# Kernel optimization log

Hardware: AMD Instinct MI355X
Metric: run time of the kernel (lower is better)

## Reference

```python
import jax, jax.numpy as jnp
import numpy as np

N, E, H, NODE_IN, EDGE_DIM, L = 10000, 400000, 128, 6, 3, 4
LN_EPS = 1e-5


def _lin_init(key, fan_in, fan_out):
    return jax.random.normal(key, (fan_in, fan_out), dtype=jnp.float32) / np.sqrt(fan_in)


def setup_inputs() -> dict:
    key = jax.random.key(0)
    ks = jax.random.split(key, 24)
    x = jax.random.normal(ks[0], (N, NODE_IN), dtype=jnp.float32)
    edge_index = jax.random.randint(ks[1], (2, E), 0, N, dtype=jnp.int64)
    edge_attr = jax.random.normal(ks[2], (E, EDGE_DIM), dtype=jnp.float32)
    # encoder
    enc_w1 = _lin_init(ks[3], NODE_IN, H); enc_b1 = jnp.zeros((H,), jnp.float32)
    enc_w2 = _lin_init(ks[4], H, H); enc_b2 = jnp.zeros((H,), jnp.float32)
    # per-layer stacked params [L, ...]
    msg_w1 = jax.vmap(lambda k: _lin_init(k, 2 * H + EDGE_DIM, H))(jax.random.split(ks[5], L))
    msg_b1 = jnp.zeros((L, H), jnp.float32)
    msg_w2 = jax.vmap(lambda k: _lin_init(k, H, H))(jax.random.split(ks[6], L))
    msg_b2 = jnp.zeros((L, H), jnp.float32)
    upd_w1 = jax.vmap(lambda k: _lin_init(k, 2 * H, H))(jax.random.split(ks[7], L))
    upd_b1 = jnp.zeros((L, H), jnp.float32)
    upd_w2 = jax.vmap(lambda k: _lin_init(k, H, H))(jax.random.split(ks[8], L))
    upd_b2 = jnp.zeros((L, H), jnp.float32)
    ln_g = jnp.ones((L, H), jnp.float32)
    ln_b = jnp.zeros((L, H), jnp.float32)
    # decoder
    dec_w1 = _lin_init(ks[9], H, H); dec_b1 = jnp.zeros((H,), jnp.float32)
    dec_w2 = _lin_init(ks[10], H, 1); dec_b2 = jnp.zeros((1,), jnp.float32)
    return dict(x=x, edge_index=edge_index, edge_attr=edge_attr,
                enc_w1=enc_w1, enc_b1=enc_b1, enc_w2=enc_w2, enc_b2=enc_b2,
                msg_w1=msg_w1, msg_b1=msg_b1, msg_w2=msg_w2, msg_b2=msg_b2,
                upd_w1=upd_w1, upd_b1=upd_b1, upd_w2=upd_w2, upd_b2=upd_b2,
                ln_g=ln_g, ln_b=ln_b,
                dec_w1=dec_w1, dec_b1=dec_b1, dec_w2=dec_w2, dec_b2=dec_b2)


def _layernorm(h, g, b):
    mu = jnp.mean(h, axis=-1, keepdims=True)
    var = jnp.mean(jnp.square(h - mu), axis=-1, keepdims=True)
    return (h - mu) * jax.lax.rsqrt(var + LN_EPS) * g + b


def reference(x, edge_index, edge_attr,
              enc_w1, enc_b1, enc_w2, enc_b2,
              msg_w1, msg_b1, msg_w2, msg_b2,
              upd_w1, upd_b1, upd_w2, upd_b2,
              ln_g, ln_b,
              dec_w1, dec_b1, dec_w2, dec_b2):
    src, tgt = edge_index[0], edge_index[1]  # PyG default flow: message from x_j=src to x_i=tgt
    # in-degree counts for mean aggregation (zero-degree nodes -> 0 output, like scatter_mean)
    counts = jax.ops.segment_sum(jnp.ones((E,), jnp.float32), tgt, num_segments=N)
    inv_counts = (1.0 / jnp.maximum(counts, 1.0))[:, None]
    # encoder
    h = jax.nn.relu(x @ enc_w1 + enc_b1) @ enc_w2 + enc_b2  # [N, H]
    for l in range(L):
        x_i = h[tgt]  # [E, H] target features
        x_j = h[src]  # [E, H] source features
        m_in = jnp.concatenate([x_i, x_j, edge_attr], axis=-1)  # [E, 2H+edge_dim]
        m = jax.nn.relu(m_in @ msg_w1[l] + msg_b1[l]) @ msg_w2[l] + msg_b2[l]  # [E, H]
        agg = jax.ops.segment_sum(m, tgt, num_segments=N) * inv_counts  # [N, H] mean aggregate
        u_in = jnp.concatenate([h, agg], axis=-1)  # [N, 2H]
        u = jax.nn.relu(u_in @ upd_w1[l] + upd_b1[l]) @ upd_w2[l] + upd_b2[l]
        h = _layernorm(u + h, ln_g[l], ln_b[l])  # residual (in==out channels)
    # decoder
    return jax.nn.relu(h @ dec_w1 + dec_b1) @ dec_w2 + dec_b2  # [N, 1]
```

## Files before the change

### kernel.cpp

```cpp
#include <hip/hip_runtime.h>

#define NN 10000
#define NE 400000
#define HD 128
#define NIN 6
#define EDIM 3
#define NL 4
#define CAP 96
#define LN_EPS 1e-5f

typedef unsigned short u16;
using short8 = __attribute__((ext_vector_type(8))) short;
using f32x4 = __attribute__((ext_vector_type(4))) float;

__device__ __forceinline__ u16 f2bf(float x) {
    unsigned u = __float_as_uint(x);
    return (u16)((u + 0x7fff + ((u >> 16) & 1)) >> 16);
}
__device__ __forceinline__ float bf2f(u16 h) { return __uint_as_float(((unsigned)h) << 16); }
__device__ __forceinline__ void split2(float x, u16& hi, u16& lo) {
    hi = f2bf(x);
    lo = f2bf(x - bf2f(hi));
}
#define MFMA(a, b, c) __builtin_amdgcn_mfma_f32_16x16x32_bf16((a), (b), (c), 0, 0, 0)


__global__ __launch_bounds__(256) void k_prepscat(
    const float* __restrict__ msg_w2, const float* __restrict__ msg_b2, const float* __restrict__ upd_w1,
    const float* __restrict__ upd_w2, const float* __restrict__ msg_w1, const float* __restrict__ dec_w1,
    const float* __restrict__ enc_w2, float* __restrict__ c2,
    u16* __restrict__ fG1, u16* __restrict__ fG2, u16* __restrict__ fPQ,
    u16* __restrict__ fDec, u16* __restrict__ fEnc,
    const int* __restrict__ srcp, const int* __restrict__ tgtp, const float* __restrict__ eattr,
    int* __restrict__ cnt, float4* __restrict__ sea) {
    if (blockIdx.x >= 442) {
        int e = (blockIdx.x - 442) * 256 + threadIdx.x;
        if (e < NE) {
            int t = tgtp[e];
            int pos = atomicAdd(&cnt[t], 1);
            if (pos < CAP) {
                sea[t * CAP + pos] = make_float4(eattr[e * 3], eattr[e * 3 + 1], eattr[e * 3 + 2],
                                                 __uint_as_float((unsigned)srcp[e]));
            }
        }
        return;
    }
    int idx = blockIdx.x * 256 + threadIdx.x;
    if (idx < 65536) {
        int l = idx >> 14, rem = idx & 16383, i = rem >> 7, jj = rem & 127;
        const float* U1b = upd_w1 + (size_t)l * 2 * HD * HD + (size_t)HD * HD;
        const float* W2 = msg_w2 + (size_t)l * HD * HD + (size_t)i * HD;
        float acc = 0.f;
        for (int t = 0; t < HD; ++t) acc += W2[t] * U1b[(size_t)t * HD + jj];
        int ct = jj >> 4;
        int ks = 4 + (i >> 5);
        int lane = (((i & 31) >> 3) << 4) | (jj & 15);
        int j = i & 7;
        int g = (l << 12) | (ct << 9) | (ks << 6) | lane;
        fG1[(size_t)g * 8 + j] = f2bf(acc);
    } else if (idx < 66048) {
        int r = idx - 65536;
        int l = r >> 7, jj = r & 127;
        const float* U1b = upd_w1 + (size_t)l * 2 * HD * HD + (size_t)HD * HD;
        const float* b2 = msg_b2 + l * HD;
        float acc = 0.f;
        for (int t = 0; t < HD; ++t) acc += b2[t] * U1b[(size_t)t * HD + jj];
        c2[r] = acc;
    } else if (idx < 76048) {
    } else if (idx < 84240) {
        int gl = idx - 76048;
        int l = gl >> 11, rem = gl & 2047;
        int ct = rem >> 8, ks = (rem >> 6) & 3, lane = rem & 63;
        int n = ct * 16 + (lane & 15), kb = ks * 32 + ((lane >> 4) << 3);
        int g = (l << 12) | (ct << 9) | (ks << 6) | lane;
        u16* dst = fG1 + (size_t)g * 8;
        const float* U = upd_w1 + (size_t)l * 256 * 128;
#pragma unroll
        for (int j = 0; j < 8; ++j) dst[j] = f2bf(U[(size_t)(kb + j) * 128 + n]);
    } else if (idx < 92432) {
        int gg = idx - 84240;
        int l = gg >> 11, r = gg & 2047;
        int ct = r >> 8, ks = (r >> 6) & 3, lane = r & 63;
        int n = ct * 16 + (lane & 15), kb = ks * 32 + ((lane >> 4) << 3);
        u16* dst = fG2 + (size_t)gg * 8;
        const float* W = upd_w2 + (size_t)l * 128 * 128;
#pragma unroll
        for (int j = 0; j < 8; ++j) dst[j] = f2bf(W[(size_t)(kb + j) * 128 + n]);
    } else if (idx < 108816) {
        int gg = idx - 92432;
        int li = gg >> 12, r = gg & 4095;
        int ct = r >> 8, ks = (r >> 6) & 3, lane = r & 63;
        int n = ct * 16 + (lane & 15), kb = ks * 32 + ((lane >> 4) << 3);
        u16* dst = fPQ + (size_t)gg * 8;
        const float* W = msg_w1 + (size_t)li * (2 * HD + EDIM) * HD;
#pragma unroll
        for (int j = 0; j < 8; ++j) {
            int k = kb + j;
            float v = (n < 128) ? W[(size_t)k * 128 + n] : W[(size_t)(128 + k) * 128 + (n - 128)];
            dst[j] = f2bf(v);
        }
    } else if (idx < 110864) {
        int r = idx - 108816;
        int ct = r >> 8, ks = (r >> 6) & 3, lane = r & 63;
        int n = ct * 16 + (lane & 15), kb = ks * 32 + ((lane >> 4) << 3);
        u16* dst = fDec + (size_t)r * 8;
#pragma unroll
        for (int j = 0; j < 8; ++j) dst[j] = f2bf(dec_w1[(size_t)(kb + j) * 128 + n]);
    } else if (idx < 112912) {
        int r = idx - 110864;
        int ct = r >> 8, ks = (r >> 6) & 3, lane = r & 63;
        int n = ct * 16 + (lane & 15), kb = ks * 32 + ((lane >> 4) << 3);
        u16* dst = fEnc + (size_t)r * 8;
#pragma unroll
        for (int j = 0; j < 8; ++j) dst[j] = f2bf(enc_w2[(size_t)(kb + j) * 128 + n]);
    }
}


__global__ __launch_bounds__(512) void k_enc(
    const float* __restrict__ x, const float* __restrict__ ew1, const float* __restrict__ eb1,
    const u16* __restrict__ fEnc, const float* __restrict__ eb2, const u16* __restrict__ fPQ0,
    const float* __restrict__ mb1, u16* __restrict__ h_hi, u16* __restrict__ h_lo,
    float* __restrict__ PQf, u16* __restrict__ Qb) {
    __shared__ u16 tHi[2048], tLo[2048];
    int tid = threadIdx.x, w = tid >> 6, lane = tid & 63, q = lane >> 4, c = lane & 15;
    int band = blockIdx.x * 16;
    {
        int col = w * 16 + c;
        float wv[NIN];
#pragma unroll
        for (int k = 0; k < NIN; ++k) wv[k] = ew1[k * HD + col];
        float ebv = eb1[col];
#pragma unroll
        for (int reg = 0; reg < 4; ++reg) {
            int row = band + q * 4 + reg;
            float t = ebv;
#pragma unroll
            for (int k = 0; k < NIN; ++k) t += x[(size_t)row * NIN + k] * wv[k];
            t = fmaxf(t, 0.f);
            u16 hi, lo;
            split2(t, hi, lo);
            int r16 = q * 4 + reg;
            int a = r16 * 128 + (((col >> 3) ^ r16) << 3) + (col & 7);
            tHi[a] = hi;
            tLo[a] = lo;
        }
    }
    __syncthreads();
    short8 aH[4], aL[4];
#pragma unroll
    for (int ks = 0; ks < 4; ++ks) {
        int a = c * 128 + (((ks * 4 + q) ^ c) << 3);
        aH[ks] = *(const short8*)&tHi[a];
        aL[ks] = *(const short8*)&tLo[a];
    }
    f32x4 acc = {0, 0, 0, 0};
    {
        const u16* fb = fEnc + (size_t)w * 4 * 512 + lane * 8;
#pragma unroll
        for (int ks = 0; ks < 4; ++ks) {
            short8 b = *(const short8*)(fb + ks * 512);
            acc = MFMA(aH[ks], b, acc);
            acc = MFMA(aL[ks], b, acc);
        }
    }
    __syncthreads();
    {
        int col = w * 16 + c;
        float ebv = eb2[col];
#pragma unroll
        for (int reg = 0; reg < 4; ++reg) {
            int r16 = q * 4 + reg, row = band + r16;
            float hval = acc[reg] + ebv;
            u16 hi, lo;
            split2(hval, hi, lo);
            h_hi[(size_t)row * HD + col] = hi;
            h_lo[(size_t)row * HD + col] = lo;
            int a = r16 * 128 + (((col >> 3) ^ r16) << 3) + (col & 7);
            tHi[a] = hi;
            tLo[a] = lo;
        }
    }
    __syncthreads();
#pragma unroll
    for (int ks = 0; ks < 4; ++ks) {
        int a = c * 128 + (((ks * 4 + q) ^ c) << 3);
        aH[ks] = *(const short8*)&tHi[a];
        aL[ks] = *(const short8*)&tLo[a];
    }
#pragma unroll
    for (int i = 0; i < 2; ++i) {
        int ctg = w * 2 + i;
        const u16* fb = fPQ0 + (size_t)ctg * 4 * 512 + lane * 8;
        f32x4 a3 = {0, 0, 0, 0};
#pragma unroll
        for (int ks = 0; ks < 4; ++ks) {
            short8 b = *(const short8*)(fb + ks * 512);
            a3 = MFMA(aH[ks], b, a3);
            a3 = MFMA(aL[ks], b, a3);
        }
        int col = ctg * 16 + c;
        if (ctg < 8) {
            float bias = mb1[col];
#pragma unroll
            for (int reg = 0; reg < 4; ++reg)
                PQf[(size_t)(band + q * 4 + reg) * HD + col] = a3[reg] + bias;
        } else {
            int colq = col - 128;
#pragma unroll
            for (int reg = 0; reg < 4; ++reg)
                Qb[(size_t)(band + q * 4 + reg) * HD + colq] = f2bf(a3[reg]);
        }
    }
}


__global__ __launch_bounds__(256) void k_gath(
    const float* __restrict__ PQf_in, const u16* __restrict__ Qb_in,
    const int* __restrict__ cnt, const float4* __restrict__ sea,
    const float* __restrict__ wc, u16* __restrict__ agg_hi, u16* __restrict__ agg_lo) {
    int w = threadIdx.x >> 6, lane = threadIdx.x & 63;
    int n = __builtin_amdgcn_readfirstlane(blockIdx.x * 4 + w);
    int cn = cnt[n];
    int cle = __builtin_amdgcn_readfirstlane(cn < CAP ? cn : CAP);
    int j = lane * 2;
    float2 p = *(const float2*)(PQf_in + (size_t)n * HD + j);
    float2 wcr0 = *(const float2*)(wc + j);
    float2 wcr1 = *(const float2*)(wc + HD + j);
    float2 wcr2 = *(const float2*)(wc + 2 * HD + j);
    const float4* bk = sea + (size_t)n * CAP;
    float acc0 = 0.f, acc1 = 0.f;
    int e = 0;
    for (; e + 16 <= cle; e += 16) {
        float4 A[16];
#pragma unroll
        for (int k = 0; k < 16; ++k) A[k] = bk[e + k];
        unsigned U[16];
#pragma unroll
        for (int k = 0; k < 16; ++k)
            U[k] = *(const unsigned*)(Qb_in + (size_t)__float_as_uint(A[k].w) * HD + j);
#pragma unroll
        for (int k = 0; k < 16; ++k) {
            float c0 = A[k].x * wcr0.x + A[k].y * wcr1.x + A[k].z * wcr2.x;
            float c1 = A[k].x * wcr0.y + A[k].y * wcr1.y + A[k].z * wcr2.y;
            acc0 += fmaxf(p.x + __uint_as_float(U[k] << 16) + c0, 0.f);
            acc1 += fmaxf(p.y + __uint_as_float(U[k] & 0xffff0000u) + c1, 0.f);
        }
    }
    int rem = cle - e;
    if (rem) {
        float4 A[16];
        unsigned U[16];
#pragma unroll
        for (int k = 0; k < 16; ++k) {
            int idx = e + (k < rem ? k : 0);
            A[k] = bk[idx];
        }
#pragma unroll
        for (int k = 0; k < 16; ++k)
            U[k] = *(const unsigned*)(Qb_in + (size_t)__float_as_uint(A[k].w) * HD + j);
#pragma unroll
        for (int k = 0; k < 16; ++k) {
            float c0 = A[k].x * wcr0.x + A[k].y * wcr1.x + A[k].z * wcr2.x;
            float c1 = A[k].x * wcr0.y + A[k].y * wcr1.y + A[k].z * wcr2.y;
            float t0 = fmaxf(p.x + __uint_as_float(U[k] << 16) + c0, 0.f);
            float t1 = fmaxf(p.y + __uint_as_float(U[k] & 0xffff0000u) + c1, 0.f);
            acc0 += (k < rem) ? t0 : 0.f;
            acc1 += (k < rem) ? t1 : 0.f;
        }
    }
    float invn = 1.0f / fmaxf((float)cn, 1.0f);
    float v0 = acc0 * invn, v1 = acc1 * invn;
    u16 h0, l0, h1, l1;
    split2(v0, h0, l0);
    split2(v1, h1, l1);
    *(ushort2*)(agg_hi + (size_t)n * HD + j) = make_ushort2(h0, h1);
    *(ushort2*)(agg_lo + (size_t)n * HD + j) = make_ushort2(l0, l1);
}


template <bool LAST>
__global__ __launch_bounds__(512) void k_layer(
    const u16* __restrict__ agg_hi, const u16* __restrict__ agg_lo, const int* __restrict__ cnt,
    u16* __restrict__ h_hi, u16* __restrict__ h_lo,
    const u16* __restrict__ fG1, const u16* __restrict__ fG2,
    const float* __restrict__ ub1, const float* __restrict__ c2l, const float* __restrict__ ub2,
    const float* __restrict__ g, const float* __restrict__ bb,
    const u16* __restrict__ fPQ, const float* __restrict__ nb1,
    float* __restrict__ PQf_out, u16* __restrict__ Qb_out,
    const u16* __restrict__ fDec, const float* __restrict__ db1, const float* __restrict__ dw2,
    const float* __restrict__ db2, float* __restrict__ out) {
    __shared__ u16 tHi[2048], tLo[2048];
    __shared__ float red[16][8][2];
    int tid = threadIdx.x, w = tid >> 6, lane = tid & 63, q = lane >> 4, c = lane & 15;
    int band = blockIdx.x * 16;
    short8 aH[8], aL[8];
    {
        size_t rb = (size_t)(band + c) * HD + q * 8;
#pragma unroll
        for (int ks = 0; ks < 4; ++ks) {
            aH[ks] = *(const short8*)(h_hi + rb + ks * 32);
            aL[ks] = *(const short8*)(h_lo + rb + ks * 32);
            aH[4 + ks] = *(const short8*)(agg_hi + rb + ks * 32);
            aL[4 + ks] = *(const short8*)(agg_lo + rb + ks * 32);
        }
    }
    f32x4 acc = {0, 0, 0, 0};
    {
        const u16* fb = fG1 + (size_t)w * 8 * 512 + lane * 8;
#pragma unroll
        for (int ks = 0; ks < 8; ++ks) {
            short8 b = *(const short8*)(fb + ks * 512);
            acc = MFMA(aH[ks], b, acc);
            acc = MFMA(aL[ks], b, acc);
        }
    }
    float alv[4];
#pragma unroll
    for (int reg = 0; reg < 4; ++reg) alv[reg] = (cnt[band + q * 4 + reg] > 0) ? 1.f : 0.f;
    {
        int col = w * 16 + c;
        float u1b = ub1[col], cc = c2l[col];
#pragma unroll
        for (int reg = 0; reg < 4; ++reg) {
            int r16 = q * 4 + reg;
            float t = fmaxf(acc[reg] + u1b + alv[reg] * cc, 0.f);
            u16 hi, lo;
            split2(t, hi, lo);
            int a = r16 * 128 + (((col >> 3) ^ r16) << 3) + (col & 7);
            tHi[a] = hi;
            tLo[a] = lo;
        }
    }
    __syncthreads();
    short8 aH2[4], aL2[4];
#pragma unroll
    for (int ks = 0; ks < 4; ++ks) {
        int a = c * 128 + (((ks * 4 + q) ^ c) << 3);
        aH2[ks] = *(const short8*)&tHi[a];
        aL2[ks] = *(const short8*)&tLo[a];
    }
    f32x4 acc2 = {0, 0, 0, 0};
    {
        const u16* fb = fG2 + (size_t)w * 4 * 512 + lane * 8;
#pragma unroll
        for (int ks = 0; ks < 4; ++ks) {
            short8 b = *(const short8*)(fb + ks * 512);
            acc2 = MFMA(aH2[ks], b, acc2);
            acc2 = MFMA(aL2[ks], b, acc2);
        }
    }
    float vv[4];
    {
        int col = w * 16 + c;
        float u2b = ub2[col];
#pragma unroll
        for (int reg = 0; reg < 4; ++reg) {
            size_t idx = (size_t)(band + q * 4 + reg) * HD + col;
            float hres = bf2f(h_hi[idx]) + bf2f(h_lo[idx]);
            vv[reg] = acc2[reg] + u2b + hres;
        }
    }
#pragma unroll
    for (int reg = 0; reg < 4; ++reg) {
        float s = vv[reg];
        float s2 = vv[reg] * vv[reg];
        for (int m = 1; m < 16; m <<= 1) {
            s += __shfl_xor(s, m);
            s2 += __shfl_xor(s2, m);
        }
        if (c == 0) {
            red[q * 4 + reg][w][0] = s;
            red[q * 4 + reg][w][1] = s2;
        }
    }
    __syncthreads();
    float mu[4], rs[4];
#pragma unroll
    for (int reg = 0; reg < 4; ++reg) {
        int r16 = q * 4 + reg;
        float S1 = 0.f, S2 = 0.f;
#pragma unroll
        for (int ww = 0; ww < 8; ++ww) {
            S1 += red[r16][ww][0];
            S2 += red[r16][ww][1];
        }
        float m = S1 * (1.f / HD);
        float var = S2 * (1.f / HD) - m * m;
        mu[reg] = m;
        rs[reg] = rsqrtf(var + LN_EPS);
    }
    {
        int col = w * 16 + c;
        float gg = g[col], bv = bb[col];
#pragma unroll
        for (int reg = 0; reg < 4; ++reg) {
            int r16 = q * 4 + reg;
            float o = (vv[reg] - mu[reg]) * rs[reg] * gg + bv;
            u16 hi, lo;
            split2(o, hi, lo);
            int a = r16 * 128 + (((col >> 3) ^ r16) << 3) + (col & 7);
            tHi[a] = hi;
            tLo[a] = lo;
            if (!LAST) {
                size_t idx = (size_t)(band + r16) * HD + col;
                h_hi[idx] = hi;
                h_lo[idx] = lo;
            }
        }
    }
    __syncthreads();
    short8 aH3[4], aL3[4];
#pragma unroll
    for (int ks = 0; ks < 4; ++ks) {
        int a = c * 128 + (((ks * 4 + q) ^ c) << 3);
        aH3[ks] = *(const short8*)&tHi[a];
        aL3[ks] = *(const short8*)&tLo[a];
    }
    if (!LAST) {
#pragma unroll
        for (int i = 0; i < 2; ++i) {
            int ctg = w * 2 + i;
            const u16* fb = fPQ + (size_t)ctg * 4 * 512 + lane * 8;
            f32x4 a3 = {0, 0, 0, 0};
#pragma unroll
            for (int ks = 0; ks < 4; ++ks) {
                short8 b = *(const short8*)(fb + ks * 512);
                a3 = MFMA(aH3[ks], b, a3);
                a3 = MFMA(aL3[ks], b, a3);
            }
            int col = ctg * 16 + c;
            if (ctg < 8) {
                float bias = nb1[col];
#pragma unroll
                for (int reg = 0; reg < 4; ++reg)
                    PQf_out[(size_t)(band + q * 4 + reg) * HD + col] = a3[reg] + bias;
            } else {
                int colq = col - 128;
#pragma unroll
                for (int reg = 0; reg < 4; ++reg)
                    Qb_out[(size_t)(band + q * 4 + reg) * HD + colq] = f2bf(a3[reg]);
            }
        }
    } else {
        float part[4];
        {
            const u16* fb = fDec + (size_t)w * 4 * 512 + lane * 8;
            f32x4 a3 = {0, 0, 0, 0};
#pragma unroll
            for (int ks = 0; ks < 4; ++ks) {
                short8 b = *(const short8*)(fb + ks * 512);
                a3 = MFMA(aH3[ks], b, a3);
                a3 = MFMA(aL3[ks], b, a3);
            }
            int col = w * 16 + c;
            float w2v = dw2[col], b1v = db1[col];
#pragma unroll
            for (int reg = 0; reg < 4; ++reg) part[reg] = fmaxf(a3[reg] + b1v, 0.f) * w2v;
        }
#pragma unroll
        for (int reg = 0; reg < 4; ++reg) {
            float s = part[reg];
            for (int m = 1; m < 16; m <<= 1) s += __shfl_xor(s, m);
            if (c == 0) red[q * 4 + reg][w][0] = s;
        }
        __syncthreads();
        if (tid < 16) {
            float s = db2[0];
#pragma unroll
            for (int ww = 0; ww < 8; ++ww) s += red[tid][ww][0];
            out[band + tid] = s;
        }
    }
}


extern "C" void kernel_launch(void* const* d_in, const int* in_sizes, int n_in,
                              void* d_out, int out_size, void* d_ws, size_t ws_size,
                              hipStream_t stream) {
    const float* x = (const float*)d_in[0];
    const int* eidx = (const int*)d_in[1];
    const float* eattr = (const float*)d_in[2];
    const float* enc_w1 = (const float*)d_in[3];
    const float* enc_b1 = (const float*)d_in[4];
    const float* enc_w2 = (const float*)d_in[5];
    const float* enc_b2 = (const float*)d_in[6];
    const float* msg_w1 = (const float*)d_in[7];
    const float* msg_b1 = (const float*)d_in[8];
    const float* msg_w2 = (const float*)d_in[9];
    const float* msg_b2 = (const float*)d_in[10];
    const float* upd_w1 = (const float*)d_in[11];
    const float* upd_b1 = (const float*)d_in[12];
    const float* upd_w2 = (const float*)d_in[13];
    const float* upd_b2 = (const float*)d_in[14];
    const float* ln_g = (const float*)d_in[15];
    const float* ln_b = (const float*)d_in[16];
    const float* dec_w1 = (const float*)d_in[17];
    const float* dec_b1 = (const float*)d_in[18];
    const float* dec_w2 = (const float*)d_in[19];
    const float* dec_b2 = (const float*)d_in[20];
    const int* srcp = eidx;
    const int* tgtp = eidx + NE;

    char* base = (char*)d_ws;
    size_t off = 0;
    auto alloc = [&](size_t bytes) -> void* {
        off = (off + 15) & ~(size_t)15;
        void* p = base + off;
        off += bytes;
        return p;
    };
    float4* sea = (float4*)alloc((size_t)NN * CAP * 16);
    float* PQf0 = (float*)alloc((size_t)NN * HD * 4);
    float* PQf1 = (float*)alloc((size_t)NN * HD * 4);
    u16* Qb0 = (u16*)alloc((size_t)NN * HD * 2);
    u16* Qb1 = (u16*)alloc((size_t)NN * HD * 2);
    u16* h_hi = (u16*)alloc((size_t)NN * HD * 2);
    u16* h_lo = (u16*)alloc((size_t)NN * HD * 2);
    u16* agg_hi = (u16*)alloc((size_t)NN * HD * 2);
    u16* agg_lo = (u16*)alloc((size_t)NN * HD * 2);
    int* cnt = (int*)alloc((size_t)NN * 4);
    float* c2 = (float*)alloc((size_t)NL * HD * 4);
    u16* fG1 = (u16*)alloc((size_t)131072 * 2);
    u16* fG2 = (u16*)alloc((size_t)65536 * 2);
    u16* fPQ = (u16*)alloc((size_t)131072 * 2);
    u16* fDec = (u16*)alloc((size_t)16384 * 2);
    u16* fEnc = (u16*)alloc((size_t)16384 * 2);

    hipMemsetAsync(cnt, 0, (size_t)NN * 4, stream);
    k_prepscat<<<442 + (NE + 255) / 256, 256, 0, stream>>>(
        msg_w2, msg_b2, upd_w1, upd_w2, msg_w1, dec_w1, enc_w2,
        c2, fG1, fG2, fPQ, fDec, fEnc,
        srcp, tgtp, eattr, cnt, sea);
    k_enc<<<625, 512, 0, stream>>>(x, enc_w1, enc_b1, fEnc, enc_b2, fPQ,
                                   msg_b1, h_hi, h_lo, PQf0, Qb0);

    float* PQin = PQf0;
    u16* Qin = Qb0;
    float* PQout = PQf1;
    u16* Qout = Qb1;
    for (int l = 0; l < NL; ++l) {
        const float* wc = msg_w1 + (size_t)l * (2 * HD + EDIM) * HD + (size_t)2 * HD * HD;
        k_gath<<<NN / 4, 256, 0, stream>>>(PQin, Qin, cnt, sea, wc, agg_hi, agg_lo);
        if (l < NL - 1) {
            k_layer<false><<<NN / 16, 512, 0, stream>>>(
                agg_hi, agg_lo, cnt, h_hi, h_lo,
                fG1 + (size_t)l * 32768, fG2 + (size_t)l * 16384,
                upd_b1 + l * HD, c2 + l * HD, upd_b2 + l * HD, ln_g + l * HD, ln_b + l * HD,
                fPQ + (size_t)(l + 1) * 32768, msg_b1 + (size_t)(l + 1) * HD, PQout, Qout,
                nullptr, nullptr, nullptr, nullptr, nullptr);
        } else {
            k_layer<true><<<NN / 16, 512, 0, stream>>>(
                agg_hi, agg_lo, cnt, h_hi, h_lo,
                fG1 + (size_t)l * 32768, fG2 + (size_t)l * 16384,
                upd_b1 + l * HD, c2 + l * HD, upd_b2 + l * HD, ln_g + l * HD, ln_b + l * HD,
                nullptr, nullptr, nullptr, nullptr,
                fDec, dec_b1, dec_w2, dec_b2, (float*)d_out);
        }
        float* tf = PQin; PQin = PQout; PQout = tf;
        u16* tq = Qin; Qin = Qout; Qout = tq;
    }
}
```

Before: 307.9 us.

## Software-pipeline edge gather loads and split MFMA accumulator chains

The gather kernel now processes edges in blocks of 8 with double-buffered register arrays. Loads and indirect Q-row fetches for the next block are issued before computing the current one, and even and odd edges go into separate accumulators. In the layer kernel, each MFMA accumulation chain is split into two independent accumulators that are summed at the end, to cut dependency stalls between back-to-back MFMAs. The cost is higher register pressure and slightly changed float summation order.

```diff
diff --git a/kernel.cpp b/kernel.cpp
--- a/kernel.cpp
+++ b/kernel.cpp
@@ -229,48 +229,63 @@
     float2 wcr1 = *(const float2*)(wc + HD + j);
     float2 wcr2 = *(const float2*)(wc + 2 * HD + j);
     const float4* bk = sea + (size_t)n * CAP;
-    float acc0 = 0.f, acc1 = 0.f;
-    int e = 0;
-    for (; e + 16 <= cle; e += 16) {
-        float4 A[16];
-#pragma unroll
-        for (int k = 0; k < 16; ++k) A[k] = bk[e + k];
-        unsigned U[16];
-#pragma unroll
-        for (int k = 0; k < 16; ++k)
+    float e0 = 0.f, e1 = 0.f, o0 = 0.f, o1 = 0.f;
+    float4 A0[8], A1[8];
+    unsigned U0[8], U1[8];
+
+    auto LA = [&](float4* A, int b) {
+#pragma unroll
+        for (int k = 0; k < 8; ++k) A[k] = bk[b * 8 + k];
+    };
+    auto IU = [&](unsigned* U, const float4* A) {
+#pragma unroll
+        for (int k = 0; k < 8; ++k)
             U[k] = *(const unsigned*)(Qb_in + (size_t)__float_as_uint(A[k].w) * HD + j);
-#pragma unroll
-        for (int k = 0; k < 16; ++k) {
-            float c0 = A[k].x * wcr0.x + A[k].y * wcr1.x + A[k].z * wcr2.x;
-            float c1 = A[k].x * wcr0.y + A[k].y * wcr1.y + A[k].z * wcr2.y;
-            acc0 += fmaxf(p.x + __uint_as_float(U[k] << 16) + c0, 0.f);
-            acc1 += fmaxf(p.y + __uint_as_float(U[k] & 0xffff0000u) + c1, 0.f);
-        }
-    }
-    int rem = cle - e;
-    if (rem) {
-        float4 A[16];
-        unsigned U[16];
-#pragma unroll
-        for (int k = 0; k < 16; ++k) {
-            int idx = e + (k < rem ? k : 0);
-            A[k] = bk[idx];
-        }
-#pragma unroll
-        for (int k = 0; k < 16; ++k)
-            U[k] = *(const unsigned*)(Qb_in + (size_t)__float_as_uint(A[k].w) * HD + j);
-#pragma unroll
-        for (int k = 0; k < 16; ++k) {
+    };
+    auto CO = [&](const float4* A, const unsigned* U) {
+#pragma unroll
+        for (int k = 0; k < 8; ++k) {
             float c0 = A[k].x * wcr0.x + A[k].y * wcr1.x + A[k].z * wcr2.x;
             float c1 = A[k].x * wcr0.y + A[k].y * wcr1.y + A[k].z * wcr2.y;
             float t0 = fmaxf(p.x + __uint_as_float(U[k] << 16) + c0, 0.f);
             float t1 = fmaxf(p.y + __uint_as_float(U[k] & 0xffff0000u) + c1, 0.f);
-            acc0 += (k < rem) ? t0 : 0.f;
-            acc1 += (k < rem) ? t1 : 0.f;
+            if (k & 1) { o0 += t0; o1 += t1; } else { e0 += t0; e1 += t1; }
+        }
+    };
+
+    int nb = cle >> 3;
+    int b = 0;
+    if (nb) {
+        LA(A0, 0);
+        IU(U0, A0);
+        for (; b + 2 <= nb; b += 2) {
+            LA(A1, b + 1);
+            IU(U1, A1);
+            CO(A0, U0);
+            if (b + 2 < nb) { LA(A0, b + 2); IU(U0, A0); }
+            CO(A1, U1);
+        }
+        if (b < nb) { CO(A0, U0); ++b; }
+    }
+    int e = nb * 8;
+    int rem = cle - e;
+    if (rem) {
+#pragma unroll
+        for (int k = 0; k < 8; ++k) A0[k] = bk[e + (k < rem ? k : 0)];
+        IU(U0, A0);
+#pragma unroll
+        for (int k = 0; k < 8; ++k) {
+            float c0 = A0[k].x * wcr0.x + A0[k].y * wcr1.x + A0[k].z * wcr2.x;
+            float c1 = A0[k].x * wcr0.y + A0[k].y * wcr1.y + A0[k].z * wcr2.y;
+            float t0 = fmaxf(p.x + __uint_as_float(U0[k] << 16) + c0, 0.f);
+            float t1 = fmaxf(p.y + __uint_as_float(U0[k] & 0xffff0000u) + c1, 0.f);
+            t0 = (k < rem) ? t0 : 0.f;
+            t1 = (k < rem) ? t1 : 0.f;
+            if (k & 1) { o0 += t0; o1 += t1; } else { e0 += t0; e1 += t1; }
         }
     }
     float invn = 1.0f / fmaxf((float)cn, 1.0f);
-    float v0 = acc0 * invn, v1 = acc1 * invn;
+    float v0 = (e0 + o0) * invn, v1 = (e1 + o1) * invn;
     u16 h0, l0, h1, l1;
     split2(v0, h0, l0);
     split2(v1, h1, l1);
@@ -305,16 +320,20 @@
             aL[4 + ks] = *(const short8*)(agg_lo + rb + ks * 32);
         }
     }
-    f32x4 acc = {0, 0, 0, 0};
+    f32x4 accA = {0, 0, 0, 0}, accB = {0, 0, 0, 0};
     {
         const u16* fb = fG1 + (size_t)w * 8 * 512 + lane * 8;
 #pragma unroll
-        for (int ks = 0; ks < 8; ++ks) {
-            short8 b = *(const short8*)(fb + ks * 512);
-            acc = MFMA(aH[ks], b, acc);
-            acc = MFMA(aL[ks], b, acc);
-        }
-    }
+        for (int ks = 0; ks < 4; ++ks) {
+            short8 bA = *(const short8*)(fb + ks * 512);
+            short8 bB = *(const short8*)(fb + (ks + 4) * 512);
+            accA = MFMA(aH[ks], bA, accA);
+            accB = MFMA(aH[ks + 4], bB, accB);
+            accA = MFMA(aL[ks], bA, accA);
+            accB = MFMA(aL[ks + 4], bB, accB);
+        }
+    }
+    f32x4 acc = accA + accB;
     float alv[4];
 #pragma unroll
     for (int reg = 0; reg < 4; ++reg) alv[reg] = (cnt[band + q * 4 + reg] > 0) ? 1.f : 0.f;
@@ -340,16 +359,20 @@
         aH2[ks] = *(const short8*)&tHi[a];
         aL2[ks] = *(const short8*)&tLo[a];
     }
-    f32x4 acc2 = {0, 0, 0, 0};
+    f32x4 acc2A = {0, 0, 0, 0}, acc2B = {0, 0, 0, 0};
     {
         const u16* fb = fG2 + (size_t)w * 4 * 512 + lane * 8;
 #pragma unroll
-        for (int ks = 0; ks < 4; ++ks) {
-            short8 b = *(const short8*)(fb + ks * 512);
-            acc2 = MFMA(aH2[ks], b, acc2);
-            acc2 = MFMA(aL2[ks], b, acc2);
-        }
-    }
+        for (int ks = 0; ks < 2; ++ks) {
+            short8 bA = *(const short8*)(fb + ks * 512);
+            short8 bB = *(const short8*)(fb + (ks + 2) * 512);
+            acc2A = MFMA(aH2[ks], bA, acc2A);
+            acc2B = MFMA(aH2[ks + 2], bB, acc2B);
+            acc2A = MFMA(aL2[ks], bA, acc2A);
+            acc2B = MFMA(aL2[ks + 2], bB, acc2B);
+        }
+    }
+    f32x4 acc2 = acc2A + acc2B;
     float vv[4];
     {
         int col = w * 16 + c;
@@ -422,13 +445,17 @@
         for (int i = 0; i < 2; ++i) {
             int ctg = w * 2 + i;
             const u16* fb = fPQ + (size_t)ctg * 4 * 512 + lane * 8;
-            f32x4 a3 = {0, 0, 0, 0};
-#pragma unroll
-            for (int ks = 0; ks < 4; ++ks) {
-                short8 b = *(const short8*)(fb + ks * 512);
-                a3 = MFMA(aH3[ks], b, a3);
-                a3 = MFMA(aL3[ks], b, a3);
+            f32x4 a3A = {0, 0, 0, 0}, a3B = {0, 0, 0, 0};
+#pragma unroll
+            for (int ks = 0; ks < 2; ++ks) {
+                short8 bA = *(const short8*)(fb + ks * 512);
+                short8 bB = *(const short8*)(fb + (ks + 2) * 512);
+                a3A = MFMA(aH3[ks], bA, a3A);
+                a3B = MFMA(aH3[ks + 2], bB, a3B);
+                a3A = MFMA(aL3[ks], bA, a3A);
+                a3B = MFMA(aL3[ks + 2], bB, a3B);
             }
+            f32x4 a3 = a3A + a3B;
             int col = ctg * 16 + c;
             if (ctg < 8) {
                 float bias = nb1[col];
@@ -446,13 +473,17 @@
         float part[4];
         {
             const u16* fb = fDec + (size_t)w * 4 * 512 + lane * 8;
-            f32x4 a3 = {0, 0, 0, 0};
-#pragma unroll
-            for (int ks = 0; ks < 4; ++ks) {
-                short8 b = *(const short8*)(fb + ks * 512);
-                a3 = MFMA(aH3[ks], b, a3);
-                a3 = MFMA(aL3[ks], b, a3);
+            f32x4 a3A = {0, 0, 0, 0}, a3B = {0, 0, 0, 0};
+#pragma unroll
+            for (int ks = 0; ks < 2; ++ks) {
+                short8 bA = *(const short8*)(fb + ks * 512);
+                short8 bB = *(const short8*)(fb + (ks + 2) * 512);
+                a3A = MFMA(aH3[ks], bA, a3A);
+                a3B = MFMA(aH3[ks + 2], bB, a3B);
+                a3A = MFMA(aL3[ks], bA, a3A);
+                a3B = MFMA(aL3[ks + 2], bB, a3B);
             }
+            f32x4 a3 = a3A + a3B;
             int col = w * 16 + c;
             float w2v = dw2[col], b1v = db1[col];
 #pragma unroll
```

New measurement: 302.5 us. No clear change (-1.7%).
